# Kernel tuning notes

Hardware: AMD Instinct MI355X
Metric: run time of the kernel (lower is better)

Reference implementation:

```python
import jax, jax.numpy as jnp
import numpy as np

N = 100000
E = 800000
IN_FEATS = 128
H_FEATS = 128
HEADS = 4
OUT = H_FEATS // HEADS  # 32
NEG_SLOPE = 0.2  # DGL GATConv default


def gat_conv(x, src, dst, W, attn_l, attn_r, bias):
    """DGL-style GATConv. x: [N, F_in] -> [N, HEADS, OUT]."""
    h = (x @ W).reshape(N, HEADS, OUT)                      # projected features
    el = jnp.sum(h * attn_l, axis=-1)                       # [N, H]
    er = jnp.sum(h * attn_r, axis=-1)                       # [N, H]
    e = jax.nn.leaky_relu(el[src] + er[dst], NEG_SLOPE)     # [E, H] edge logits
    # edge softmax over incoming edges of each dst node
    m = jax.ops.segment_max(e, dst, num_segments=N)          # [N, H]
    ex = jnp.exp(e - m[dst])                                 # [E, H]
    s = jax.ops.segment_sum(ex, dst, num_segments=N)         # [N, H]
    a = ex / s[dst]                                          # [E, H]
    msg = h[src] * a[:, :, None]                             # [E, H, OUT]
    out = jax.ops.segment_sum(msg, dst, num_segments=N)      # [N, H, OUT]
    return out + bias.reshape(1, HEADS, OUT)


def setup_inputs() -> dict:
    key = jax.random.key(0)
    ks = jax.random.split(key, 12)
    feat = jax.random.normal(ks[0], (N, IN_FEATS), dtype=jnp.float32)
    src = jax.random.randint(ks[1], (E,), 0, N)
    dst = jax.random.randint(ks[2], (E,), 0, N)
    s1 = 1.0 / np.sqrt(IN_FEATS)
    s2 = 1.0 / np.sqrt(H_FEATS)
    return {
        "feat": feat,
        "src": src,
        "dst": dst,
        "W1": jax.random.normal(ks[3], (IN_FEATS, HEADS * OUT), dtype=jnp.float32) * s1,
        "al1": jax.random.normal(ks[4], (HEADS, OUT), dtype=jnp.float32) * s2,
        "ar1": jax.random.normal(ks[5], (HEADS, OUT), dtype=jnp.float32) * s2,
        "b1": jnp.zeros((HEADS * OUT,), dtype=jnp.float32),
        "W2": jax.random.normal(ks[6], (H_FEATS, HEADS * OUT), dtype=jnp.float32) * s2,
        "al2": jax.random.normal(ks[7], (HEADS, OUT), dtype=jnp.float32) * s2,
        "ar2": jax.random.normal(ks[8], (HEADS, OUT), dtype=jnp.float32) * s2,
        "b2": jnp.zeros((HEADS * OUT,), dtype=jnp.float32),
    }


def reference(feat, src, dst, W1, al1, ar1, b1, W2, al2, ar2, b2):
    h = gat_conv(feat, src, dst, W1, al1, ar1, b1).reshape(N, H_FEATS)  # flatten(1)
    h = jax.nn.relu(h)
    h = gat_conv(h, src, dst, W2, al2, ar2, b2).mean(axis=1)            # mean over heads
    return h
```

## Files before the change

### kernel.cpp

```cpp
#include <hip/hip_runtime.h>
#include <math.h>

#define N_NODES 100000
#define N_EDGES 800000
#define NEG_SLOPE 0.2f
#define NB_CSR 98
#define NT_CSR (NB_CSR * 256)

typedef __attribute__((ext_vector_type(8))) short short8;
typedef __attribute__((ext_vector_type(4))) float floatx4;

__device__ __forceinline__ float lrelu(float x) { return x > 0.f ? x : NEG_SLOPE * x; }

__device__ __forceinline__ unsigned bf16_rne(float f) {
    unsigned u = __float_as_uint(f);
    return (u + 0x7fffu + ((u >> 16) & 1u)) >> 16;
}
__device__ __forceinline__ unsigned bfpack(float lo, float hi) {
    return bf16_rne(lo) | (bf16_rne(hi) << 16);
}
__device__ __forceinline__ float bflo(unsigned p) { return __uint_as_float(p << 16); }
__device__ __forceinline__ float bfhi(unsigned p) { return __uint_as_float(p & 0xffff0000u); }

__device__ __forceinline__ void gbar(int* ctr) {
    __syncthreads();
    if (threadIdx.x == 0) {
        __threadfence();
        atomicAdd(ctr, 1);
        while (atomicAdd(ctr, 0) < NB_CSR) { }
    }
    __syncthreads();
}

__global__ __launch_bounds__(256) void k_pre(const int* __restrict__ src,
                                             const int* __restrict__ dst,
                                             int* __restrict__ deg,
                                             int* __restrict__ rs,
                                             int* __restrict__ cursor,
                                             int* __restrict__ bsums,
                                             int* __restrict__ done,
                                             int* __restrict__ csr_src,
                                             const float* __restrict__ W1,
                                             const float* __restrict__ al1,
                                             const float* __restrict__ ar1,
                                             const float* __restrict__ W2,
                                             const float* __restrict__ al2,
                                             const float* __restrict__ ar2,
                                             unsigned short* __restrict__ wt1,
                                             unsigned short* __restrict__ wt2,
                                             unsigned short* __restrict__ et1,
                                             unsigned short* __restrict__ et2) {
    int b = blockIdx.x, tid = threadIdx.x;
    if (b >= NB_CSR) {
        int wb = b - NB_CSR;
        if (wb < 128) {
            int t2 = wb * 256 + tid;
            const float* W = (t2 < 16384) ? W1 : W2;
            unsigned short* wt = (t2 < 16384) ? wt1 : wt2;
            int t = t2 & 16383;
            int n = t >> 7, k = t & 127;
            wt[t] = (unsigned short)bf16_rne(W[k * 128 + n]);
        } else {
            const float* W = (wb == 128) ? W1 : W2;
            const float* al = (wb == 128) ? al1 : al2;
            const float* ar = (wb == 128) ? ar1 : ar2;
            unsigned short* et = (wb == 128) ? et1 : et2;
            for (int o = tid * 8; o < tid * 8 + 8; o++) {
                int n = o >> 7, k = o & 127;
                float sacc = 0.f;
                if (n < 8) {
                    const float* a = (n < 4) ? al : ar;
                    int hh = n & 3;
                    #pragma unroll 8
                    for (int c = 0; c < 32; c++)
                        sacc += W[k * 128 + hh * 32 + c] * a[hh * 32 + c];
                }
                et[n * 128 + k] = (unsigned short)bf16_rne(sacc);
            }
        }
        return;
    }

    int gtid = b * 256 + tid;
    for (int i = gtid; i < N_NODES; i += NT_CSR) deg[i] = 0;
    gbar(&done[0]);
    for (int e = gtid; e < N_EDGES; e += NT_CSR) atomicAdd(&deg[dst[e]], 1);
    gbar(&done[1]);
    __shared__ int sd[256];
    int base = b * 1024 + tid * 4;
    int v0 = (base + 0 < N_NODES) ? atomicAdd(&deg[base + 0], 0) : 0;
    int v1 = (base + 1 < N_NODES) ? atomicAdd(&deg[base + 1], 0) : 0;
    int v2 = (base + 2 < N_NODES) ? atomicAdd(&deg[base + 2], 0) : 0;
    int v3 = (base + 3 < N_NODES) ? atomicAdd(&deg[base + 3], 0) : 0;
    int t = v0 + v1 + v2 + v3;
    sd[tid] = t;
    __syncthreads();
    int incl = t;
    for (int off = 1; off < 256; off <<= 1) {
        int x = (tid >= off) ? sd[tid - off] : 0;
        __syncthreads();
        incl += x;
        sd[tid] = incl;
        __syncthreads();
    }
    int excl = incl - t;

    if (tid == 255) {
        atomicExch(&bsums[b], incl);
        __threadfence();
        atomicAdd(&done[2], 1);
    }
    if (tid == 0) {
        while (atomicAdd(&done[2], 0) < NB_CSR) { }
    }
    __syncthreads();

    int bv = (tid < b) ? atomicAdd(&bsums[tid], 0) : 0;
    __syncthreads();
    sd[tid] = bv;
    __syncthreads();
    for (int off = 128; off > 0; off >>= 1) {
        if (tid < off) sd[tid] += sd[tid + off];
        __syncthreads();
    }
    int boff = sd[0];

    int p0 = excl + boff;
    if (base + 0 < N_NODES) { rs[base + 0] = p0; cursor[base + 0] = p0; }
    if (base + 1 < N_NODES) { rs[base + 1] = p0 + v0; cursor[base + 1] = p0 + v0; }
    if (base + 2 < N_NODES) { rs[base + 2] = p0 + v0 + v1; cursor[base + 2] = p0 + v0 + v1; }
    if (base + 3 < N_NODES) { rs[base + 3] = p0 + v0 + v1 + v2; cursor[base + 3] = p0 + v0 + v1 + v2; }
    if (b == 0 && tid == 0) rs[N_NODES] = N_EDGES;
    gbar(&done[3]);
    for (int e = gtid; e < N_EDGES; e += NT_CSR) {
        int d = dst[e];
        int p = atomicAdd(&cursor[d], 1);
        csr_src[p] = src[e];
    }
}

__global__ __launch_bounds__(256) void k_gemm(const void* __restrict__ Xv,
                                              const unsigned short* __restrict__ wt,
                                              const unsigned short* __restrict__ et,
                                              unsigned* __restrict__ Hb,
                                              float* __restrict__ EL,
                                              float* __restrict__ ER,
                                              int src_bf16) {
    __shared__ unsigned short wsh[128 * 128];
    __shared__ unsigned short esh[16 * 136];
    int tid = threadIdx.x;
    int w = tid >> 6, lane = tid & 63;
    int q = lane >> 4, nl = lane & 15;
    int base = blockIdx.x * 128;

    const uint4* wt4 = (const uint4*)wt;
    #pragma unroll
    for (int i = 0; i < 8; i++) {
        int idx = tid + i * 256;
        int rn = idx >> 4, c8 = idx & 15;
        int kc = c8 >> 2, qq = c8 & 3;
        int slot = rn * 128 + ((kc ^ ((rn >> 2) & 3)) * 4 + (qq ^ (rn & 3))) * 8;
        *(uint4*)&wsh[slot] = wt4[idx];
    }
    {
        const uint4* et4 = (const uint4*)et;
        int rn = tid >> 4, c8 = tid & 15;
        *(uint4*)&esh[rn * 136 + c8 * 8] = et4[tid];
    }

    short8 afr[2][4];
    int row0 = base + w * 32 + nl;
    if (!src_bf16) {
        const float4* X4 = (const float4*)Xv;
        #pragma unroll
        for (int rt = 0; rt < 2; rt++) {
            int rr = row0 + rt * 16; if (rr > N_NODES - 1) rr = N_NODES - 1;
            const float4* px = X4 + (size_t)rr * 32 + q * 2;
            #pragma unroll
            for (int kc = 0; kc < 4; kc++) {
                float4 u = px[kc * 8], v = px[kc * 8 + 1];
                short8 f;
                f[0] = (short)bf16_rne(u.x); f[1] = (short)bf16_rne(u.y);
                f[2] = (short)bf16_rne(u.z); f[3] = (short)bf16_rne(u.w);
                f[4] = (short)bf16_rne(v.x); f[5] = (short)bf16_rne(v.y);
                f[6] = (short)bf16_rne(v.z); f[7] = (short)bf16_rne(v.w);
                afr[rt][kc] = f;
            }
        }
    } else {
        const unsigned short* Xb = (const unsigned short*)Xv;
        #pragma unroll
        for (int rt = 0; rt < 2; rt++) {
            int rr = row0 + rt * 16; if (rr > N_NODES - 1) rr = N_NODES - 1;
            #pragma unroll
            for (int kc = 0; kc < 4; kc++)
                afr[rt][kc] = *(const short8*)(Xb + (size_t)rr * 128 + kc * 32 + q * 8);
        }
    }

    floatx4 acc[2][8];
    floatx4 acc_e[2];
    #pragma unroll
    for (int rt = 0; rt < 2; rt++) {
        acc_e[rt] = (floatx4){0.f, 0.f, 0.f, 0.f};
        #pragma unroll
        for (int ct = 0; ct < 8; ct++)
            acc[rt][ct] = (floatx4){0.f, 0.f, 0.f, 0.f};
    }

    __syncthreads();

    int sw_hi = (nl >> 2) & 3, sw_lo = nl & 3;
    #pragma unroll
    for (int ct = 0; ct < 8; ct++) {
        int rbase = (ct * 16 + nl) * 128;
        #pragma unroll
        for (int kc = 0; kc < 4; kc++) {
            short8 b = *(const short8*)&wsh[rbase + ((kc ^ sw_hi) * 4 + (q ^ sw_lo)) * 8];
            acc[0][ct] = __builtin_amdgcn_mfma_f32_16x16x32_bf16(afr[0][kc], b, acc[0][ct], 0, 0, 0);
            acc[1][ct] = __builtin_amdgcn_mfma_f32_16x16x32_bf16(afr[1][kc], b, acc[1][ct], 0, 0, 0);
        }
    }
    #pragma unroll
    for (int kc = 0; kc < 4; kc++) {
        short8 e8 = *(const short8*)&esh[nl * 136 + (kc * 4 + q) * 8];
        acc_e[0] = __builtin_amdgcn_mfma_f32_16x16x32_bf16(afr[0][kc], e8, acc_e[0], 0, 0, 0);
        acc_e[1] = __builtin_amdgcn_mfma_f32_16x16x32_bf16(afr[1][kc], e8, acc_e[1], 0, 0, 0);
    }

    #pragma unroll
    for (int rt = 0; rt < 2; rt++) {
        #pragma unroll
        for (int r = 0; r < 4; r++) {
            int row = base + w * 32 + rt * 16 + q * 4 + r;
            bool valid = row < N_NODES;
            unsigned* hrow = Hb + (size_t)row * 64;
            #pragma unroll
            for (int ct = 0; ct < 8; ct++) {
                float vlo = acc[rt][ct][r];
                float vhi = __shfl_down(vlo, 1);
                if (valid && !(nl & 1)) hrow[ct * 8 + (nl >> 1)] = bfpack(vlo, vhi);
            }
            if (valid && nl < 8) {
                float v = acc_e[rt][r];
                if (nl < 4) EL[row * 4 + nl] = v;
                else        ER[row * 4 + (nl & 3)] = v;
            }
        }
    }
}

__global__ __launch_bounds__(256) void k_gather(const int* __restrict__ rs,
                                                const int* __restrict__ csr_src,
                                                const float* __restrict__ EL,
                                                const float* __restrict__ ER,
                                                const unsigned* __restrict__ Hb,
                                                const float* __restrict__ bias,
                                                void* __restrict__ out,
                                                int final_layer) {
    int wid = (blockIdx.x * blockDim.x + threadIdx.x) >> 6;
    int lane = threadIdx.x & 63;
    int g = lane >> 4, l16 = lane & 15;
    int h = l16 >> 2;
    int n0 = wid * 4;
    if (n0 >= N_NODES) return;
    int nend = min(n0 + 4, N_NODES);

    float bv[8];
    #pragma unroll
    for (int c = 0; c < 8; c++) bv[c] = bias[l16 * 8 + c];

    for (int n = n0; n < nend; n++) {
        int s = rs[n], e = rs[n + 1];
        float erh = ER[n * 4 + h];
        float acc[8];
        #pragma unroll
        for (int c = 0; c < 8; c++) acc[c] = 0.f;
        float sa = 0.f;

        for (int j = s; j < e; j += 8) {
            int j0 = j + g, j1 = j + 4 + g;
            uint4 p0 = make_uint4(0, 0, 0, 0), p1 = make_uint4(0, 0, 0, 0);
            float w0 = 0.f, w1 = 0.f;
            if (j0 < e) {
                int s0 = csr_src[j0];
                p0 = *(const uint4*)(Hb + (size_t)s0 * 64 + l16 * 4);
                w0 = __expf(lrelu(EL[s0 * 4 + h] + erh));
            }
            if (j1 < e) {
                int s1 = csr_src[j1];
                p1 = *(const uint4*)(Hb + (size_t)s1 * 64 + l16 * 4);
                w1 = __expf(lrelu(EL[s1 * 4 + h] + erh));
            }
            sa += w0 + w1;
            acc[0] = fmaf(bflo(p0.x), w0, acc[0]); acc[1] = fmaf(bfhi(p0.x), w0, acc[1]);
            acc[2] = fmaf(bflo(p0.y), w0, acc[2]); acc[3] = fmaf(bfhi(p0.y), w0, acc[3]);
            acc[4] = fmaf(bflo(p0.z), w0, acc[4]); acc[5] = fmaf(bfhi(p0.z), w0, acc[5]);
            acc[6] = fmaf(bflo(p0.w), w0, acc[6]); acc[7] = fmaf(bfhi(p0.w), w0, acc[7]);
            acc[0] = fmaf(bflo(p1.x), w1, acc[0]); acc[1] = fmaf(bfhi(p1.x), w1, acc[1]);
            acc[2] = fmaf(bflo(p1.y), w1, acc[2]); acc[3] = fmaf(bfhi(p1.y), w1, acc[3]);
            acc[4] = fmaf(bflo(p1.z), w1, acc[4]); acc[5] = fmaf(bfhi(p1.z), w1, acc[5]);
            acc[6] = fmaf(bflo(p1.w), w1, acc[6]); acc[7] = fmaf(bfhi(p1.w), w1, acc[7]);
        }

        #pragma unroll
        for (int c = 0; c < 8; c++) {
            acc[c] += __shfl_xor(acc[c], 16);
            acc[c] += __shfl_xor(acc[c], 32);
        }
        sa += __shfl_xor(sa, 16);
        sa += __shfl_xor(sa, 32);
        float inv = (e > s) ? 1.f / sa : 0.f;

        float r[8];
        #pragma unroll
        for (int c = 0; c < 8; c++) r[c] = acc[c] * inv + bv[c];

        if (!final_layer) {
            if (g == 0) {
                uint4 pk;
                pk.x = bfpack(fmaxf(r[0], 0.f), fmaxf(r[1], 0.f));
                pk.y = bfpack(fmaxf(r[2], 0.f), fmaxf(r[3], 0.f));
                pk.z = bfpack(fmaxf(r[4], 0.f), fmaxf(r[5], 0.f));
                pk.w = bfpack(fmaxf(r[6], 0.f), fmaxf(r[7], 0.f));
                *(uint4*)((unsigned*)out + (size_t)n * 64 + l16 * 4) = pk;
            }
        } else {
            #pragma unroll
            for (int c = 0; c < 8; c++) {
                r[c] += __shfl_xor(r[c], 4);
                r[c] += __shfl_xor(r[c], 8);
            }
            if (g == 0 && l16 < 4) {
                float* po = (float*)out + (size_t)n * 32 + l16 * 8;
                *(float4*)po = make_float4(0.25f * r[0], 0.25f * r[1], 0.25f * r[2], 0.25f * r[3]);
                *(float4*)(po + 4) = make_float4(0.25f * r[4], 0.25f * r[5], 0.25f * r[6], 0.25f * r[7]);
            }
        }
    }
}

extern "C" void kernel_launch(void* const* d_in, const int* in_sizes, int n_in,
                              void* d_out, int out_size, void* d_ws, size_t ws_size,
                              hipStream_t stream) {
    const float* feat = (const float*)d_in[0];
    const int* src = (const int*)d_in[1];
    const int* dst = (const int*)d_in[2];
    const float* W1 = (const float*)d_in[3];
    const float* al1 = (const float*)d_in[4];
    const float* ar1 = (const float*)d_in[5];
    const float* b1 = (const float*)d_in[6];
    const float* W2 = (const float*)d_in[7];
    const float* al2 = (const float*)d_in[8];
    const float* ar2 = (const float*)d_in[9];
    const float* b2 = (const float*)d_in[10];
    float* out = (float*)d_out;

    char* ws = (char*)d_ws;
    size_t off = 0;
    auto alloc = [&](size_t bytes) {
        void* p = ws + off;
        off += (bytes + 255) & ~(size_t)255;
        return p;
    };
    int* done = (int*)alloc(256);
    int* deg = (int*)alloc((size_t)N_NODES * 4);
    int* rs = (int*)alloc(((size_t)N_NODES + 1) * 4);
    int* cursor = (int*)alloc((size_t)N_NODES * 4);
    int* bsums = (int*)alloc(128 * 4);
    int* csr_src = (int*)alloc((size_t)N_EDGES * 4);
    unsigned* Hb = (unsigned*)alloc((size_t)N_NODES * 64 * 4);
    float* el = (float*)alloc((size_t)N_NODES * 4 * 4);
    float* er = (float*)alloc((size_t)N_NODES * 4 * 4);
    unsigned* out1b = (unsigned*)alloc((size_t)N_NODES * 64 * 4);
    unsigned short* wt1 = (unsigned short*)alloc(128 * 128 * 2);
    unsigned short* wt2 = (unsigned short*)alloc(128 * 128 * 2);
    unsigned short* et1 = (unsigned short*)alloc(16 * 128 * 2);
    unsigned short* et2 = (unsigned short*)alloc(16 * 128 * 2);

    hipMemsetAsync(done, 0, 256, stream);

    k_pre<<<NB_CSR + 128 + 2, 256, 0, stream>>>(src, dst, deg, rs, cursor, bsums, done,
                                                csr_src, W1, al1, ar1, W2, al2, ar2,
                                                wt1, wt2, et1, et2);

    int gemm_blocks = (N_NODES + 127) / 128;
    int gat_blocks = (N_NODES + 15) / 16;

    k_gemm<<<gemm_blocks, 256, 0, stream>>>(feat, wt1, et1, Hb, el, er, 0);
    k_gather<<<gat_blocks, 256, 0, stream>>>(rs, csr_src, el, er, Hb, b1, out1b, 0);
    k_gemm<<<gemm_blocks, 256, 0, stream>>>(out1b, wt2, et2, Hb, el, er, 1);
    k_gather<<<gat_blocks, 256, 0, stream>>>(rs, csr_src, el, er, Hb, b2, out, 1);
}
```

Measured before the change: 330.8 us.

## Split persistent CSR-build kernel into separate histogram, scan, and scatter launches

Replaces the single 98-block persistent kernel, which used spin-wait grid barriers between its phases, with three kernels: a full-grid histogram plus weight prep, a 98-block scan that keeps one cross-block spin wait, and a full-grid scatter. The degree array is now zeroed by the memset instead of a kernel phase, and the scan reads degrees with plain loads instead of atomics. The goal is to spread edge atomics over many more blocks and drop the global barrier spins, in exchange for two extra kernel launches.

```diff
diff --git a/kernel.cpp b/kernel.cpp
--- a/kernel.cpp
+++ b/kernel.cpp
@@ -4,8 +4,6 @@
 #define N_NODES 100000
 #define N_EDGES 800000
 #define NEG_SLOPE 0.2f
-#define NB_CSR 98
-#define NT_CSR (NB_CSR * 256)
 
 typedef __attribute__((ext_vector_type(8))) short short8;
 typedef __attribute__((ext_vector_type(4))) float floatx4;
@@ -22,76 +20,61 @@
 __device__ __forceinline__ float bflo(unsigned p) { return __uint_as_float(p << 16); }
 __device__ __forceinline__ float bfhi(unsigned p) { return __uint_as_float(p & 0xffff0000u); }
 
-__device__ __forceinline__ void gbar(int* ctr) {
-    __syncthreads();
-    if (threadIdx.x == 0) {
-        __threadfence();
-        atomicAdd(ctr, 1);
-        while (atomicAdd(ctr, 0) < NB_CSR) { }
-    }
-    __syncthreads();
-}
-
-__global__ __launch_bounds__(256) void k_pre(const int* __restrict__ src,
-                                             const int* __restrict__ dst,
-                                             int* __restrict__ deg,
-                                             int* __restrict__ rs,
-                                             int* __restrict__ cursor,
-                                             int* __restrict__ bsums,
-                                             int* __restrict__ done,
-                                             int* __restrict__ csr_src,
-                                             const float* __restrict__ W1,
-                                             const float* __restrict__ al1,
-                                             const float* __restrict__ ar1,
-                                             const float* __restrict__ W2,
-                                             const float* __restrict__ al2,
-                                             const float* __restrict__ ar2,
-                                             unsigned short* __restrict__ wt1,
-                                             unsigned short* __restrict__ wt2,
-                                             unsigned short* __restrict__ et1,
-                                             unsigned short* __restrict__ et2) {
+__global__ __launch_bounds__(256) void k_hist_wprep(const int* __restrict__ dst,
+                                                    int* __restrict__ deg,
+                                                    const float* __restrict__ W1,
+                                                    const float* __restrict__ al1,
+                                                    const float* __restrict__ ar1,
+                                                    const float* __restrict__ W2,
+                                                    const float* __restrict__ al2,
+                                                    const float* __restrict__ ar2,
+                                                    unsigned short* __restrict__ wt1,
+                                                    unsigned short* __restrict__ wt2,
+                                                    unsigned short* __restrict__ et1,
+                                                    unsigned short* __restrict__ et2) {
     int b = blockIdx.x, tid = threadIdx.x;
-    if (b >= NB_CSR) {
-        int wb = b - NB_CSR;
-        if (wb < 128) {
-            int t2 = wb * 256 + tid;
-            const float* W = (t2 < 16384) ? W1 : W2;
-            unsigned short* wt = (t2 < 16384) ? wt1 : wt2;
-            int t = t2 & 16383;
-            int n = t >> 7, k = t & 127;
-            wt[t] = (unsigned short)bf16_rne(W[k * 128 + n]);
-        } else {
-            const float* W = (wb == 128) ? W1 : W2;
-            const float* al = (wb == 128) ? al1 : al2;
-            const float* ar = (wb == 128) ? ar1 : ar2;
-            unsigned short* et = (wb == 128) ? et1 : et2;
-            for (int o = tid * 8; o < tid * 8 + 8; o++) {
-                int n = o >> 7, k = o & 127;
-                float sacc = 0.f;
-                if (n < 8) {
-                    const float* a = (n < 4) ? al : ar;
-                    int hh = n & 3;
-                    #pragma unroll 8
-                    for (int c = 0; c < 32; c++)
-                        sacc += W[k * 128 + hh * 32 + c] * a[hh * 32 + c];
-                }
-                et[n * 128 + k] = (unsigned short)bf16_rne(sacc);
-            }
-        }
-        return;
-    }
-
-    int gtid = b * 256 + tid;
-    for (int i = gtid; i < N_NODES; i += NT_CSR) deg[i] = 0;
-    gbar(&done[0]);
-    for (int e = gtid; e < N_EDGES; e += NT_CSR) atomicAdd(&deg[dst[e]], 1);
-    gbar(&done[1]);
+    if (b < 3125) {
+        int e = b * 256 + tid;
+        if (e < N_EDGES) atomicAdd(&deg[dst[e]], 1);
+    } else if (b < 3253) {
+        int t2 = (b - 3125) * 256 + tid;
+        const float* W = (t2 < 16384) ? W1 : W2;
+        unsigned short* wt = (t2 < 16384) ? wt1 : wt2;
+        int t = t2 & 16383;
+        int n = t >> 7, k = t & 127;
+        wt[t] = (unsigned short)bf16_rne(W[k * 128 + n]);
+    } else {
+        const float* W = (b == 3253) ? W1 : W2;
+        const float* al = (b == 3253) ? al1 : al2;
+        const float* ar = (b == 3253) ? ar1 : ar2;
+        unsigned short* et = (b == 3253) ? et1 : et2;
+        for (int o = tid * 8; o < tid * 8 + 8; o++) {
+            int n = o >> 7, k = o & 127;
+            float sacc = 0.f;
+            if (n < 8) {
+                const float* a = (n < 4) ? al : ar;
+                int hh = n & 3;
+                #pragma unroll 8
+                for (int c = 0; c < 32; c++)
+                    sacc += W[k * 128 + hh * 32 + c] * a[hh * 32 + c];
+            }
+            et[n * 128 + k] = (unsigned short)bf16_rne(sacc);
+        }
+    }
+}
+
+__global__ __launch_bounds__(256) void k_scan(const int* __restrict__ deg,
+                                              int* __restrict__ rs,
+                                              int* __restrict__ cursor,
+                                              int* __restrict__ bsums,
+                                              int* __restrict__ done) {
     __shared__ int sd[256];
+    int tid = threadIdx.x, b = blockIdx.x;
     int base = b * 1024 + tid * 4;
-    int v0 = (base + 0 < N_NODES) ? atomicAdd(&deg[base + 0], 0) : 0;
-    int v1 = (base + 1 < N_NODES) ? atomicAdd(&deg[base + 1], 0) : 0;
-    int v2 = (base + 2 < N_NODES) ? atomicAdd(&deg[base + 2], 0) : 0;
-    int v3 = (base + 3 < N_NODES) ? atomicAdd(&deg[base + 3], 0) : 0;
+    int v0 = (base + 0 < N_NODES) ? deg[base + 0] : 0;
+    int v1 = (base + 1 < N_NODES) ? deg[base + 1] : 0;
+    int v2 = (base + 2 < N_NODES) ? deg[base + 2] : 0;
+    int v3 = (base + 3 < N_NODES) ? deg[base + 3] : 0;
     int t = v0 + v1 + v2 + v3;
     sd[tid] = t;
     __syncthreads();
@@ -108,10 +91,10 @@
     if (tid == 255) {
         atomicExch(&bsums[b], incl);
         __threadfence();
-        atomicAdd(&done[2], 1);
+        atomicAdd(done, 1);
     }
     if (tid == 0) {
-        while (atomicAdd(&done[2], 0) < NB_CSR) { }
+        while (atomicAdd(done, 0) < 98) { }
     }
     __syncthreads();
 
@@ -131,8 +114,12 @@
     if (base + 2 < N_NODES) { rs[base + 2] = p0 + v0 + v1; cursor[base + 2] = p0 + v0 + v1; }
     if (base + 3 < N_NODES) { rs[base + 3] = p0 + v0 + v1 + v2; cursor[base + 3] = p0 + v0 + v1 + v2; }
     if (b == 0 && tid == 0) rs[N_NODES] = N_EDGES;
-    gbar(&done[3]);
-    for (int e = gtid; e < N_EDGES; e += NT_CSR) {
+}
+
+__global__ void k_scatter(const int* __restrict__ src, const int* __restrict__ dst,
+                          int* __restrict__ cursor, int* __restrict__ csr_src) {
+    int e = blockIdx.x * blockDim.x + threadIdx.x;
+    if (e < N_EDGES) {
         int d = dst[e];
         int p = atomicAdd(&cursor[d], 1);
         csr_src[p] = src[e];
@@ -363,8 +350,8 @@
         off += (bytes + 255) & ~(size_t)255;
         return p;
     };
+    int* deg = (int*)alloc((size_t)N_NODES * 4);
     int* done = (int*)alloc(256);
-    int* deg = (int*)alloc((size_t)N_NODES * 4);
     int* rs = (int*)alloc(((size_t)N_NODES + 1) * 4);
     int* cursor = (int*)alloc((size_t)N_NODES * 4);
     int* bsums = (int*)alloc(128 * 4);
@@ -378,11 +365,13 @@
     unsigned short* et1 = (unsigned short*)alloc(16 * 128 * 2);
     unsigned short* et2 = (unsigned short*)alloc(16 * 128 * 2);
 
-    hipMemsetAsync(done, 0, 256, stream);
-
-    k_pre<<<NB_CSR + 128 + 2, 256, 0, stream>>>(src, dst, deg, rs, cursor, bsums, done,
-                                                csr_src, W1, al1, ar1, W2, al2, ar2,
-                                                wt1, wt2, et1, et2);
+    size_t zbytes = (size_t)((char*)done - (char*)deg) + 256;
+    hipMemsetAsync(deg, 0, zbytes, stream);
+
+    k_hist_wprep<<<3125 + 128 + 2, 256, 0, stream>>>(dst, deg, W1, al1, ar1,
+                                                     W2, al2, ar2, wt1, wt2, et1, et2);
+    k_scan<<<98, 256, 0, stream>>>(deg, rs, cursor, bsums, done);
+    k_scatter<<<(N_EDGES + 255) / 256, 256, 0, stream>>>(src, dst, cursor, csr_src);
 
     int gemm_blocks = (N_NODES + 127) / 128;
     int gat_blocks = (N_NODES + 15) / 16;
```

After: 330.1 us. No clear change (-0.2%).
